# Kernel tuning notes

Hardware: AMD Instinct MI355X
Metric: run time of the kernel (lower is better)

## Reference

```python
import jax, jax.numpy as jnp
import numpy as np

HID = 16   # hidden_dim
K = 16     # kNN neighbors
B = 64     # graphs per batch
N_TS = 8192
N_LC = 12288


def setup_inputs() -> dict:
    key = jax.random.key(0)
    ks = jax.random.split(key, 24)

    def lin(k, fan_in, fan_out):
        w = jax.random.normal(k, (fan_in, fan_out), jnp.float32) / np.sqrt(fan_in).astype(np.float32)
        return w

    inp = {
        "x_ts": jax.random.normal(ks[0], (N_TS, 6), jnp.float32),
        "x_lc": jax.random.normal(ks[1], (N_LC, 5), jnp.float32),
        # balanced sorted graph ids -> every graph has >= K source nodes
        "batch_ts": jnp.repeat(jnp.arange(B, dtype=jnp.int32), N_TS // B),
        "batch_lc": jnp.repeat(jnp.arange(B, dtype=jnp.int32), N_LC // B),
        # ts_encode: Linear(6,16), ELU, Linear(16,16), ELU
        "ts_w1": lin(ks[2], 6, HID),  "ts_b1": jnp.zeros((HID,), jnp.float32),
        "ts_w2": lin(ks[3], HID, HID), "ts_b2": jnp.zeros((HID,), jnp.float32),
        # lc_encode: Linear(5,16), ELU, Linear(16,16), ELU
        "lc_w1": lin(ks[4], 5, HID),  "lc_b1": jnp.zeros((HID,), jnp.float32),
        "lc_w2": lin(ks[5], HID, HID), "lc_b2": jnp.zeros((HID,), jnp.float32),
        # EdgeConv nn: Linear(2*16, 16), ELU  (shared across the 3 conv calls)
        "conv_w": lin(ks[6], 2 * HID, HID), "conv_b": jnp.zeros((HID,), jnp.float32),
        # output MLP 16->64->32->8->4->1 (ELU between, none after last)
        "out_w1": lin(ks[7], HID, 64), "out_b1": jnp.zeros((64,), jnp.float32),
        "out_w2": lin(ks[8], 64, 32),  "out_b2": jnp.zeros((32,), jnp.float32),
        "out_w3": lin(ks[9], 32, 8),   "out_b3": jnp.zeros((8,), jnp.float32),
        "out_w4": lin(ks[10], 8, 4),   "out_b4": jnp.zeros((4,), jnp.float32),
        "out_w5": lin(ks[11], 4, 1),   "out_b5": jnp.zeros((1,), jnp.float32),
    }
    return inp


def _mlp2(x, w1, b1, w2, b2):
    return jax.nn.elu(jax.nn.elu(x @ w1 + b1) @ w2 + b2)


def _edge_conv(x_src, x_dst, b_src, b_dst, w, b):
    """DynamicEdgeConv: per-graph kNN of dst queries into src, message
    nn(cat[x_i, x_j - x_i]), max-aggregate over the K neighbors."""
    # squared distances [N_dst, N_src]
    d2 = (jnp.sum(x_dst * x_dst, 1)[:, None]
          - 2.0 * (x_dst @ x_src.T)
          + jnp.sum(x_src * x_src, 1)[None, :])
    d2 = jnp.where(b_dst[:, None] == b_src[None, :], d2, jnp.inf)
    _, idx = jax.lax.top_k(-d2, K)          # [N_dst, K] nearest (incl. self when src==dst)
    xj = x_src[idx]                          # [N_dst, K, H] gather
    xi = x_dst[:, None, :]                   # [N_dst, 1, H]
    msg = jnp.concatenate([jnp.broadcast_to(xi, xj.shape), xj - xi], axis=-1)
    msg = jax.nn.elu(msg @ w + b)            # [N_dst, K, H]
    return jnp.max(msg, axis=1)              # max aggregation -> [N_dst, H]


def reference(x_ts, x_lc, batch_ts, batch_lc,
              ts_w1, ts_b1, ts_w2, ts_b2,
              lc_w1, lc_b1, lc_w2, lc_b2,
              conv_w, conv_b,
              out_w1, out_b1, out_w2, out_b2, out_w3, out_b3,
              out_w4, out_b4, out_w5, out_b5):
    x_ts_enc = _mlp2(x_ts, ts_w1, ts_b1, ts_w2, ts_b2)   # [N_ts, 16]
    x_lc_enc = _mlp2(x_lc, lc_w1, lc_b1, lc_w2, lc_b2)   # [N_lc, 16]

    feats1 = _edge_conv(x_lc_enc, x_lc_enc, batch_lc, batch_lc, conv_w, conv_b)  # [N_lc,16]
    feats2 = _edge_conv(x_lc_enc, x_ts_enc, batch_lc, batch_ts, conv_w, conv_b)  # [N_ts,16]
    feats3 = _edge_conv(feats1,   feats2,   batch_lc, batch_ts, conv_w, conv_b)  # [N_ts,16]

    # avg_pool_x(batch_ts, feats3, batch_ts): per-graph mean
    sums = jax.ops.segment_sum(feats3, batch_ts, num_segments=B)
    cnts = jax.ops.segment_sum(jnp.ones((feats3.shape[0],), feats3.dtype), batch_ts, num_segments=B)
    pooled = sums / cnts[:, None]                         # [B, 16]

    h = jax.nn.elu(pooled @ out_w1 + out_b1)
    h = jax.nn.elu(h @ out_w2 + out_b2)
    h = jax.nn.elu(h @ out_w3 + out_b3)
    h = jax.nn.elu(h @ out_w4 + out_b4)
    out = h @ out_w5 + out_b5                             # [B, 1]
    batch_out = jnp.arange(B, dtype=batch_ts.dtype)
    return (out, batch_out)
```

## Files before the change

kernel.cpp:

```cpp
#include <hip/hip_runtime.h>
#include <math.h>

#define HID 16
#define KNN 16
#define NB 64
#define NTS 8192
#define NLC 12288
#define TSG 128
#define LCG 192

__device__ __forceinline__ float eluf(float x) {
    return x > 0.0f ? x : expm1f(x);
}

__device__ __forceinline__ unsigned int f2ord(float f) {
    unsigned int b = __float_as_uint(f);
    return b ^ (((int)b >> 31) | 0x80000000u);
}

__global__ __launch_bounds__(256) void encode_kernel(
    const float* __restrict__ x_ts, const float* __restrict__ x_lc,
    const float* __restrict__ ts_w1, const float* __restrict__ ts_b1,
    const float* __restrict__ ts_w2, const float* __restrict__ ts_b2,
    const float* __restrict__ lc_w1, const float* __restrict__ lc_b1,
    const float* __restrict__ lc_w2, const float* __restrict__ lc_b2,
    const float* __restrict__ cw,
    float* __restrict__ ts_enc, float* __restrict__ lc_enc,
    float* __restrict__ y_lc, float* __restrict__ n_lc,
    float* __restrict__ pooled)
{
    __shared__ float sw1[6 * HID];
    __shared__ float sw2[HID * HID];
    __shared__ float scw2[HID * HID];
    __shared__ float sb1[HID];
    __shared__ float sb2[HID];
    __shared__ float s_h[64 * 17];

    const int tid = threadIdx.x;
    const int t = blockIdx.x * 256 + tid;
    if (t < NB * HID) pooled[t] = 0.0f;

    const bool is_ts = (blockIdx.x < NTS / 64);
    const float* w1 = is_ts ? ts_w1 : lc_w1;
    const float* b1 = is_ts ? ts_b1 : lc_b1;
    const float* w2 = is_ts ? ts_w2 : lc_w2;
    const float* b2 = is_ts ? ts_b2 : lc_b2;
    const int in_dim = is_ts ? 6 : 5;

    if (tid < in_dim * HID) sw1[tid] = w1[tid];
    if (tid < HID * HID)    sw2[tid] = w2[tid];
    if (!is_ts && tid < HID * HID) scw2[tid] = cw[HID * HID + tid];
    if (tid < HID)          { sb1[tid] = b1[tid]; sb2[tid] = b2[tid]; }
    __syncthreads();

    const int q    = tid & 3;
    const int rloc = tid >> 2;
    const int row  = is_ts ? (blockIdx.x * 64 + rloc)
                           : ((blockIdx.x - 128) * 64 + rloc);
    const float* x = is_ts ? (x_ts + (size_t)row * 6) : (x_lc + (size_t)row * 5);
    float* outp    = is_ts ? (ts_enc + (size_t)row * HID) : (lc_enc + (size_t)row * HID);

    float xin[6];
    for (int k = 0; k < in_dim; ++k) xin[k] = x[k];

    #pragma unroll
    for (int jc = 0; jc < 4; ++jc) {
        const int c = 4 * q + jc;
        float s = sb1[c];
        for (int k = 0; k < in_dim; ++k) s += xin[k] * sw1[k * HID + c];
        s_h[rloc * 17 + c] = eluf(s);
    }
    __syncthreads();
    float hf[HID];
    #pragma unroll
    for (int k = 0; k < HID; ++k) hf[k] = s_h[rloc * 17 + k];

    float o4v[4];
    #pragma unroll
    for (int jc = 0; jc < 4; ++jc) {
        const int c = 4 * q + jc;
        float s = sb2[c];
        #pragma unroll
        for (int k = 0; k < HID; ++k) s += hf[k] * sw2[k * HID + c];
        o4v[jc] = eluf(s);
    }
    reinterpret_cast<float4*>(outp)[q] = make_float4(o4v[0], o4v[1], o4v[2], o4v[3]);

    if (!is_ts) {
        __syncthreads();
        #pragma unroll
        for (int jc = 0; jc < 4; ++jc) s_h[rloc * 17 + 4 * q + jc] = o4v[jc];
        __syncthreads();
        float of[HID];
        #pragma unroll
        for (int k = 0; k < HID; ++k) of[k] = s_h[rloc * 17 + k];
        float nv = 0.f;
        #pragma unroll
        for (int c = 0; c < HID; ++c) nv += of[c] * of[c];
        float y4[4];
        #pragma unroll
        for (int jc = 0; jc < 4; ++jc) {
            const int c = 4 * q + jc;
            float s = 0.f;
            #pragma unroll
            for (int k = 0; k < HID; ++k) s += of[k] * scw2[k * HID + c];
            y4[jc] = s;
        }
        reinterpret_cast<float4*>(y_lc + (size_t)row * HID)[q] =
            make_float4(y4[0], y4[1], y4[2], y4[3]);
        if (q == 0) n_lc[row] = nv;
    }
}

#define CONV_SMEM_FLOATS (LCG * HID + 2 * HID * HID + 2 * HID)
#define CONV_SMEM_BYTES  (CONV_SMEM_FLOATS * 4)

template<int NSRC, int NDST, bool POOL, bool EPI, bool SELF>
__device__ __forceinline__ void edgeconv_impl(
    float* __restrict__ smem, int bid,
    const float* __restrict__ src, const float* __restrict__ src_y,
    const float* __restrict__ src_n, const float* __restrict__ dst,
    const float* __restrict__ cw, const float* __restrict__ cb,
    float* __restrict__ out_feats, float* __restrict__ out_y,
    float* __restrict__ out_n, float* __restrict__ pool_out)
{
    constexpr int RPW = 2;
    constexpr int RPB = 8 * RPW;
    constexpr int BPG = NDST / RPB;
    float* s_y    = smem;
    float* s_dw   = s_y + NSRC * HID;
    float* s_w2   = s_dw + HID * HID;
    float* s_b    = s_w2 + HID * HID;
    float* s_pool = s_b + HID;

    const int tid  = threadIdx.x;
    const int lane = tid & 63;
    const int wave = tid >> 6;
    const int g      = bid / BPG;
    const int rowblk = bid % BPG;

    if (tid < HID * HID) {
        float w1v = cw[tid];
        float w2v = cw[HID * HID + tid];
        s_dw[tid] = w1v - w2v;
        if (EPI) s_w2[tid] = w2v;
    }
    if (tid < HID) s_b[tid] = cb[tid];
    if (POOL && tid < HID) s_pool[tid] = 0.0f;
    {
        const float4* gy = reinterpret_cast<const float4*>(src_y + (size_t)(g * NSRC) * HID);
        float4* sy4 = reinterpret_cast<float4*>(s_y);
        for (int i = tid; i < NSRC * HID / 4; i += 512) sy4[i] = gy[i];
    }

    float rw[3][HID];
    float rn[3];
    #pragma unroll
    for (int k = 0; k < 3; ++k) {
        const float4* rp = reinterpret_cast<const float4*>(src + (size_t)(g * NSRC + lane + 64 * k) * HID);
        float4 a = rp[0], b = rp[1], c4 = rp[2], e = rp[3];
        rw[k][0] = a.x;  rw[k][1] = a.y;  rw[k][2]  = a.z;  rw[k][3]  = a.w;
        rw[k][4] = b.x;  rw[k][5] = b.y;  rw[k][6]  = b.z;  rw[k][7]  = b.w;
        rw[k][8] = c4.x; rw[k][9] = c4.y; rw[k][10] = c4.z; rw[k][11] = c4.w;
        rw[k][12] = e.x; rw[k][13] = e.y; rw[k][14] = e.z;  rw[k][15] = e.w;
        rn[k] = src_n[g * NSRC + lane + 64 * k];
    }

    const int drow0 = rowblk * RPB + wave * RPW;
    const int c = lane & 15;

    for (int r2 = 0; r2 < RPW; ++r2) {
        const int drow = drow0 + r2;

        const float4* d4 = reinterpret_cast<const float4*>(dst + (size_t)(g * NDST + drow) * HID);
        float xi[HID];
        {
            float4 a = d4[0], b = d4[1], c4 = d4[2], e = d4[3];
            xi[0] = a.x;  xi[1] = a.y;  xi[2]  = a.z;  xi[3]  = a.w;
            xi[4] = b.x;  xi[5] = b.y;  xi[6]  = b.z;  xi[7]  = b.w;
            xi[8] = c4.x; xi[9] = c4.y; xi[10] = c4.z; xi[11] = c4.w;
            xi[12] = e.x; xi[13] = e.y; xi[14] = e.z;  xi[15] = e.w;
        }
        float nd;
        if (SELF) {
            nd = src_n[g * NSRC + drow];
        } else {
            float s = 0.f;
            #pragma unroll
            for (int cc = 0; cc < HID; ++cc) s += xi[cc] * xi[cc];
            nd = s;
        }

        unsigned int dk0, dk1, dk2;
        {
            unsigned int dk[3];
            #pragma unroll
            for (int k = 0; k < 3; ++k) {
                float dot = 0.f;
                #pragma unroll
                for (int cc = 0; cc < HID; ++cc) dot += xi[cc] * rw[k][cc];
                dk[k] = f2ord(nd - 2.0f * dot + rn[k]);
            }
            dk0 = dk[0]; dk1 = dk[1]; dk2 = dk[2];
        }

        unsigned int p = 0;
        int k = KNN;
        int cls = 3 * 64;
        int b = 31;
        for (; b >= 0; --b) {
            if (cls == k) break;
            unsigned int pb = p >> b;
            int cnt = __popcll(__ballot((dk0 >> b) == pb))
                    + __popcll(__ballot((dk1 >> b) == pb))
                    + __popcll(__ballot((dk2 >> b) == pb));
            if (k > cnt) { k -= cnt; p |= (1u << b); cls -= cnt; }
            else cls = cnt;
        }
        unsigned int qi = 255u;
        if (b >= 0) {
            p |= (1u << (b + 1)) - 1u;
        } else if (cls != k) {
            qi = 0;
            int kk = k;
            const unsigned int i0 = (unsigned)lane, i1 = (unsigned)(lane + 64), i2 = (unsigned)(lane + 128);
            for (int bb = 7; bb >= 0; --bb) {
                unsigned int qb = qi >> bb;
                int cnt = __popcll(__ballot(dk0 == p && (i0 >> bb) == qb))
                        + __popcll(__ballot(dk1 == p && (i1 >> bb) == qb))
                        + __popcll(__ballot(dk2 == p && (i2 >> bb) == qb));
                if (kk > cnt) { kk -= cnt; qi |= (1u << bb); }
            }
        }
        unsigned long long m0 = __ballot(dk0 < p || (dk0 == p && (unsigned)lane <= qi));
        unsigned long long m1 = __ballot(dk1 < p || (dk1 == p && (unsigned)(lane + 64) <= qi));
        unsigned long long m2 = __ballot(dk2 < p || (dk2 == p && (unsigned)(lane + 128) <= qi));

        if (r2 == 0) __syncthreads();

        float cic = s_b[c];
        #pragma unroll
        for (int r = 0; r < HID; ++r) cic += xi[r] * s_dw[r * HID + c];

        int jarr[KNN];
        #pragma unroll
        for (int i = 0; i < KNN; ++i) {
            int j;
            if (m0)      { j = __builtin_ctzll(m0);       m0 &= m0 - 1; }
            else if (m1) { j = 64 + __builtin_ctzll(m1);  m1 &= m1 - 1; }
            else         { j = 128 + __builtin_ctzll(m2); m2 &= m2 - 1; }
            jarr[i] = j;
        }
        float yv[KNN];
        #pragma unroll
        for (int i = 0; i < KNN; ++i) yv[i] = s_y[jarr[i] * HID + c];
        float ym = yv[0];
        #pragma unroll
        for (int i = 1; i < KNN; ++i) ym = fmaxf(ym, yv[i]);

        const float f = eluf(cic + ym);

        if (POOL) {
            if (lane < HID) atomicAdd(&s_pool[c], f);
        } else {
            const int grow = g * NDST + drow;
            if (lane < HID) out_feats[(size_t)grow * HID + c] = f;
            if (EPI) {
                float yvv = 0.f, nv = 0.f;
                #pragma unroll
                for (int r = 0; r < HID; ++r) {
                    float fr = __shfl(f, r, 64);
                    yvv += fr * s_w2[r * HID + c];
                    nv += fr * fr;
                }
                if (lane < HID) out_y[(size_t)grow * HID + c] = yvv;
                if (lane == 0)  out_n[grow] = nv;
            }
        }
    }

    if (POOL) {
        __syncthreads();
        if (tid < HID) atomicAdd(&pool_out[g * HID + tid], s_pool[tid]);
    }
}

#define C1_BLOCKS (NB * (LCG / 16))
#define C2_BLOCKS (NB * (TSG / 16))
__global__ __launch_bounds__(512) void edgeconv12_kernel(
    const float* __restrict__ lc_enc, const float* __restrict__ y_lc,
    const float* __restrict__ n_lc, const float* __restrict__ ts_enc,
    const float* __restrict__ cw, const float* __restrict__ cb,
    float* __restrict__ feats1, float* __restrict__ y_f1, float* __restrict__ n_f1,
    float* __restrict__ feats2)
{
    extern __shared__ float smem[];
    if (blockIdx.x < C1_BLOCKS)
        edgeconv_impl<LCG, LCG, false, true, true>(smem, blockIdx.x, lc_enc, y_lc, n_lc,
                                                   lc_enc, cw, cb, feats1, y_f1, n_f1, nullptr);
    else
        edgeconv_impl<LCG, TSG, false, false, false>(smem, blockIdx.x - C1_BLOCKS, lc_enc, y_lc, n_lc,
                                                     ts_enc, cw, cb, feats2, nullptr, nullptr, nullptr);
}

__global__ __launch_bounds__(512) void edgeconv3_kernel(
    const float* __restrict__ feats1, const float* __restrict__ y_f1,
    const float* __restrict__ n_f1, const float* __restrict__ feats2,
    const float* __restrict__ cw, const float* __restrict__ cb,
    float* __restrict__ pooled)
{
    extern __shared__ float smem[];
    edgeconv_impl<LCG, TSG, true, false, false>(smem, blockIdx.x, feats1, y_f1, n_f1,
                                                feats2, cw, cb, nullptr, nullptr, nullptr, pooled);
}

__global__ __launch_bounds__(64) void head_kernel(
    const float* __restrict__ pooled,
    const float* __restrict__ w1, const float* __restrict__ b1,
    const float* __restrict__ w2, const float* __restrict__ b2,
    const float* __restrict__ w3, const float* __restrict__ b3,
    const float* __restrict__ w4, const float* __restrict__ b4,
    const float* __restrict__ w5, const float* __restrict__ b5,
    float* __restrict__ out)
{
    const int g = blockIdx.x;
    const int lane = threadIdx.x;
    __shared__ float sp[HID];
    __shared__ float sh1[64];
    __shared__ float sh2[32];
    __shared__ float sh3[8];
    __shared__ float sh4[4];

    if (lane < HID) sp[lane] = pooled[g * HID + lane] * (1.0f / (float)TSG);
    __syncthreads();

    {
        float s = b1[lane];
        #pragma unroll
        for (int r = 0; r < HID; ++r) s += sp[r] * w1[r * 64 + lane];
        sh1[lane] = eluf(s);
    }
    __syncthreads();
    if (lane < 32) {
        float s = b2[lane];
        #pragma unroll
        for (int r = 0; r < 64; ++r) s += sh1[r] * w2[r * 32 + lane];
        sh2[lane] = eluf(s);
    }
    __syncthreads();
    if (lane < 8) {
        float s = b3[lane];
        #pragma unroll
        for (int r = 0; r < 32; ++r) s += sh2[r] * w3[r * 8 + lane];
        sh3[lane] = eluf(s);
    }
    __syncthreads();
    if (lane < 4) {
        float s = b4[lane];
        #pragma unroll
        for (int r = 0; r < 8; ++r) s += sh3[r] * w4[r * 4 + lane];
        sh4[lane] = eluf(s);
    }
    __syncthreads();
    if (lane == 0) {
        float s = b5[0];
        #pragma unroll
        for (int r = 0; r < 4; ++r) s += sh4[r] * w5[r];
        out[g] = s;
        out[NB + g] = (float)g;
    }
}

extern "C" void kernel_launch(void* const* d_in, const int* in_sizes, int n_in,
                              void* d_out, int out_size, void* d_ws, size_t ws_size,
                              hipStream_t stream) {
    const float* x_ts  = (const float*)d_in[0];
    const float* x_lc  = (const float*)d_in[1];
    const float* ts_w1 = (const float*)d_in[4];
    const float* ts_b1 = (const float*)d_in[5];
    const float* ts_w2 = (const float*)d_in[6];
    const float* ts_b2 = (const float*)d_in[7];
    const float* lc_w1 = (const float*)d_in[8];
    const float* lc_b1 = (const float*)d_in[9];
    const float* lc_w2 = (const float*)d_in[10];
    const float* lc_b2 = (const float*)d_in[11];
    const float* cw    = (const float*)d_in[12];
    const float* cb    = (const float*)d_in[13];
    const float* ow1   = (const float*)d_in[14];
    const float* ob1   = (const float*)d_in[15];
    const float* ow2   = (const float*)d_in[16];
    const float* ob2   = (const float*)d_in[17];
    const float* ow3   = (const float*)d_in[18];
    const float* ob3   = (const float*)d_in[19];
    const float* ow4   = (const float*)d_in[20];
    const float* ob4   = (const float*)d_in[21];
    const float* ow5   = (const float*)d_in[22];
    const float* ob5   = (const float*)d_in[23];
    float* out = (float*)d_out;

    float* ws = (float*)d_ws;
    float* ts_enc = ws;
    float* lc_enc = ws + 131072;
    float* feats1 = ws + 327680;
    float* feats2 = ws + 524288;
    float* pooled = ws + 655360;
    float* y_lc   = ws + 656384;
    float* n_lc   = ws + 852992;
    float* y_f1   = ws + 865280;
    float* n_f1   = ws + 1061888;

    encode_kernel<<<(NTS + NLC) / 64, 256, 0, stream>>>(
        x_ts, x_lc, ts_w1, ts_b1, ts_w2, ts_b2, lc_w1, lc_b1, lc_w2, lc_b2,
        cw, ts_enc, lc_enc, y_lc, n_lc, pooled);

    edgeconv12_kernel<<<C1_BLOCKS + C2_BLOCKS, 512, CONV_SMEM_BYTES, stream>>>(
        lc_enc, y_lc, n_lc, ts_enc, cw, cb, feats1, y_f1, n_f1, feats2);

    edgeconv3_kernel<<<C2_BLOCKS, 512, CONV_SMEM_BYTES, stream>>>(
        feats1, y_f1, n_f1, feats2, cw, cb, pooled);

    head_kernel<<<NB, 64, 0, stream>>>(
        pooled, ow1, ob1, ow2, ob2, ow3, ob3, ow4, ob4, ow5, ob5, out);
}
```

Baseline: 156.1 us.

## Fuse node encoders into edgeconv kernel, recomputing per-graph encodings in shared memory

Drops the separate encode kernel. Each edgeconv block for convs 1 and 2 now recomputes its graph's 192 lc encodings (plus norms and y projections) and its 16 ts destination rows directly into shared memory, then runs kNN from shared memory. This removes one launch and the global round-trip of the encoded features, at the cost of redundant encoder work: every one of the 12 or 8 blocks per graph recomputes the same lc encodings. Conv3 is unrolled into its own specialized kernel, and the pooled buffer is now zeroed by block 0.

```diff
diff --git a/kernel.cpp b/kernel.cpp
--- a/kernel.cpp
+++ b/kernel.cpp
@@ -18,120 +18,35 @@
     return b ^ (((int)b >> 31) | 0x80000000u);
 }
 
-__global__ __launch_bounds__(256) void encode_kernel(
+
+struct FusedSmem {
+    float enc[LCG * 17];
+    float y[LCG * 17];
+    float n[LCG];
+    float dw[HID * HID];
+    float cw2[HID * HID];
+    float b[HID];
+    float w1lc[5 * HID]; float b1lc[HID]; float w2lc[HID * HID]; float b2lc[HID];
+    float w1ts[6 * HID]; float b1ts[HID]; float w2ts[HID * HID]; float b2ts[HID];
+    float dst[16 * 17];
+};
+
+template<bool IS_C1>
+__device__ __forceinline__ void fused_impl(
+    FusedSmem& sm, int bid,
     const float* __restrict__ x_ts, const float* __restrict__ x_lc,
     const float* __restrict__ ts_w1, const float* __restrict__ ts_b1,
     const float* __restrict__ ts_w2, const float* __restrict__ ts_b2,
     const float* __restrict__ lc_w1, const float* __restrict__ lc_b1,
     const float* __restrict__ lc_w2, const float* __restrict__ lc_b2,
-    const float* __restrict__ cw,
-    float* __restrict__ ts_enc, float* __restrict__ lc_enc,
-    float* __restrict__ y_lc, float* __restrict__ n_lc,
-    float* __restrict__ pooled)
-{
-    __shared__ float sw1[6 * HID];
-    __shared__ float sw2[HID * HID];
-    __shared__ float scw2[HID * HID];
-    __shared__ float sb1[HID];
-    __shared__ float sb2[HID];
-    __shared__ float s_h[64 * 17];
-
-    const int tid = threadIdx.x;
-    const int t = blockIdx.x * 256 + tid;
-    if (t < NB * HID) pooled[t] = 0.0f;
-
-    const bool is_ts = (blockIdx.x < NTS / 64);
-    const float* w1 = is_ts ? ts_w1 : lc_w1;
-    const float* b1 = is_ts ? ts_b1 : lc_b1;
-    const float* w2 = is_ts ? ts_w2 : lc_w2;
-    const float* b2 = is_ts ? ts_b2 : lc_b2;
-    const int in_dim = is_ts ? 6 : 5;
-
-    if (tid < in_dim * HID) sw1[tid] = w1[tid];
-    if (tid < HID * HID)    sw2[tid] = w2[tid];
-    if (!is_ts && tid < HID * HID) scw2[tid] = cw[HID * HID + tid];
-    if (tid < HID)          { sb1[tid] = b1[tid]; sb2[tid] = b2[tid]; }
-    __syncthreads();
-
-    const int q    = tid & 3;
-    const int rloc = tid >> 2;
-    const int row  = is_ts ? (blockIdx.x * 64 + rloc)
-                           : ((blockIdx.x - 128) * 64 + rloc);
-    const float* x = is_ts ? (x_ts + (size_t)row * 6) : (x_lc + (size_t)row * 5);
-    float* outp    = is_ts ? (ts_enc + (size_t)row * HID) : (lc_enc + (size_t)row * HID);
-
-    float xin[6];
-    for (int k = 0; k < in_dim; ++k) xin[k] = x[k];
-
-    #pragma unroll
-    for (int jc = 0; jc < 4; ++jc) {
-        const int c = 4 * q + jc;
-        float s = sb1[c];
-        for (int k = 0; k < in_dim; ++k) s += xin[k] * sw1[k * HID + c];
-        s_h[rloc * 17 + c] = eluf(s);
-    }
-    __syncthreads();
-    float hf[HID];
-    #pragma unroll
-    for (int k = 0; k < HID; ++k) hf[k] = s_h[rloc * 17 + k];
-
-    float o4v[4];
-    #pragma unroll
-    for (int jc = 0; jc < 4; ++jc) {
-        const int c = 4 * q + jc;
-        float s = sb2[c];
-        #pragma unroll
-        for (int k = 0; k < HID; ++k) s += hf[k] * sw2[k * HID + c];
-        o4v[jc] = eluf(s);
-    }
-    reinterpret_cast<float4*>(outp)[q] = make_float4(o4v[0], o4v[1], o4v[2], o4v[3]);
-
-    if (!is_ts) {
-        __syncthreads();
-        #pragma unroll
-        for (int jc = 0; jc < 4; ++jc) s_h[rloc * 17 + 4 * q + jc] = o4v[jc];
-        __syncthreads();
-        float of[HID];
-        #pragma unroll
-        for (int k = 0; k < HID; ++k) of[k] = s_h[rloc * 17 + k];
-        float nv = 0.f;
-        #pragma unroll
-        for (int c = 0; c < HID; ++c) nv += of[c] * of[c];
-        float y4[4];
-        #pragma unroll
-        for (int jc = 0; jc < 4; ++jc) {
-            const int c = 4 * q + jc;
-            float s = 0.f;
-            #pragma unroll
-            for (int k = 0; k < HID; ++k) s += of[k] * scw2[k * HID + c];
-            y4[jc] = s;
-        }
-        reinterpret_cast<float4*>(y_lc + (size_t)row * HID)[q] =
-            make_float4(y4[0], y4[1], y4[2], y4[3]);
-        if (q == 0) n_lc[row] = nv;
-    }
-}
-
-#define CONV_SMEM_FLOATS (LCG * HID + 2 * HID * HID + 2 * HID)
-#define CONV_SMEM_BYTES  (CONV_SMEM_FLOATS * 4)
-
-template<int NSRC, int NDST, bool POOL, bool EPI, bool SELF>
-__device__ __forceinline__ void edgeconv_impl(
-    float* __restrict__ smem, int bid,
-    const float* __restrict__ src, const float* __restrict__ src_y,
-    const float* __restrict__ src_n, const float* __restrict__ dst,
     const float* __restrict__ cw, const float* __restrict__ cb,
     float* __restrict__ out_feats, float* __restrict__ out_y,
-    float* __restrict__ out_n, float* __restrict__ pool_out)
+    float* __restrict__ out_n)
 {
+    constexpr int NDST = IS_C1 ? LCG : TSG;
     constexpr int RPW = 2;
     constexpr int RPB = 8 * RPW;
     constexpr int BPG = NDST / RPB;
-    float* s_y    = smem;
-    float* s_dw   = s_y + NSRC * HID;
-    float* s_w2   = s_dw + HID * HID;
-    float* s_b    = s_w2 + HID * HID;
-    float* s_pool = s_b + HID;
 
     const int tid  = threadIdx.x;
     const int lane = tid & 63;
@@ -140,30 +55,86 @@
     const int rowblk = bid % BPG;
 
     if (tid < HID * HID) {
-        float w1v = cw[tid];
-        float w2v = cw[HID * HID + tid];
-        s_dw[tid] = w1v - w2v;
-        if (EPI) s_w2[tid] = w2v;
-    }
-    if (tid < HID) s_b[tid] = cb[tid];
-    if (POOL && tid < HID) s_pool[tid] = 0.0f;
-    {
-        const float4* gy = reinterpret_cast<const float4*>(src_y + (size_t)(g * NSRC) * HID);
-        float4* sy4 = reinterpret_cast<float4*>(s_y);
-        for (int i = tid; i < NSRC * HID / 4; i += 512) sy4[i] = gy[i];
-    }
+        float w1v = cw[tid], w2v = cw[HID * HID + tid];
+        sm.dw[tid]  = w1v - w2v;
+        sm.cw2[tid] = w2v;
+        sm.w2lc[tid] = lc_w2[tid];
+        if (!IS_C1) sm.w2ts[tid] = ts_w2[tid];
+    }
+    if (tid < 5 * HID) sm.w1lc[tid] = lc_w1[tid];
+    if (!IS_C1 && tid < 6 * HID) sm.w1ts[tid] = ts_w1[tid];
+    if (tid < HID) {
+        sm.b1lc[tid] = lc_b1[tid]; sm.b2lc[tid] = lc_b2[tid]; sm.b[tid] = cb[tid];
+        if (!IS_C1) { sm.b1ts[tid] = ts_b1[tid]; sm.b2ts[tid] = ts_b2[tid]; }
+    }
+    __syncthreads();
+
+    if (tid < LCG) {
+        const int r = tid;
+        const float* xp = x_lc + (size_t)(g * LCG + r) * 5;
+        float xin[5];
+        #pragma unroll
+        for (int k = 0; k < 5; ++k) xin[k] = xp[k];
+        float h[HID];
+        #pragma unroll
+        for (int c = 0; c < HID; ++c) {
+            float s = sm.b1lc[c];
+            #pragma unroll
+            for (int k = 0; k < 5; ++k) s += xin[k] * sm.w1lc[k * HID + c];
+            h[c] = eluf(s);
+        }
+        float o[HID];
+        #pragma unroll
+        for (int c = 0; c < HID; ++c) {
+            float s = sm.b2lc[c];
+            #pragma unroll
+            for (int k = 0; k < HID; ++k) s += h[k] * sm.w2lc[k * HID + c];
+            o[c] = eluf(s);
+            sm.enc[r * 17 + c] = o[c];
+        }
+        float nv = 0.f;
+        #pragma unroll
+        for (int c = 0; c < HID; ++c) nv += o[c] * o[c];
+        sm.n[r] = nv;
+        #pragma unroll
+        for (int c = 0; c < HID; ++c) {
+            float s = 0.f;
+            #pragma unroll
+            for (int k = 0; k < HID; ++k) s += o[k] * sm.cw2[k * HID + c];
+            sm.y[r * 17 + c] = s;
+        }
+    }
+    if (!IS_C1 && tid >= LCG && tid < LCG + 16) {
+        const int i = tid - LCG;
+        const float* xp = x_ts + (size_t)(g * TSG + rowblk * 16 + i) * 6;
+        float xin[6];
+        #pragma unroll
+        for (int k = 0; k < 6; ++k) xin[k] = xp[k];
+        float h[HID];
+        #pragma unroll
+        for (int c = 0; c < HID; ++c) {
+            float s = sm.b1ts[c];
+            #pragma unroll
+            for (int k = 0; k < 6; ++k) s += xin[k] * sm.w1ts[k * HID + c];
+            h[c] = eluf(s);
+        }
+        #pragma unroll
+        for (int c = 0; c < HID; ++c) {
+            float s = sm.b2ts[c];
+            #pragma unroll
+            for (int k = 0; k < HID; ++k) s += h[k] * sm.w2ts[k * HID + c];
+            sm.dst[i * 17 + c] = eluf(s);
+        }
+    }
+    __syncthreads();
 
     float rw[3][HID];
     float rn[3];
     #pragma unroll
     for (int k = 0; k < 3; ++k) {
-        const float4* rp = reinterpret_cast<const float4*>(src + (size_t)(g * NSRC + lane + 64 * k) * HID);
-        float4 a = rp[0], b = rp[1], c4 = rp[2], e = rp[3];
-        rw[k][0] = a.x;  rw[k][1] = a.y;  rw[k][2]  = a.z;  rw[k][3]  = a.w;
-        rw[k][4] = b.x;  rw[k][5] = b.y;  rw[k][6]  = b.z;  rw[k][7]  = b.w;
-        rw[k][8] = c4.x; rw[k][9] = c4.y; rw[k][10] = c4.z; rw[k][11] = c4.w;
-        rw[k][12] = e.x; rw[k][13] = e.y; rw[k][14] = e.z;  rw[k][15] = e.w;
-        rn[k] = src_n[g * NSRC + lane + 64 * k];
+        #pragma unroll
+        for (int c = 0; c < HID; ++c) rw[k][c] = sm.enc[(lane + 64 * k) * 17 + c];
+        rn[k] = sm.n[lane + 64 * k];
     }
 
     const int drow0 = rowblk * RPB + wave * RPW;
@@ -172,18 +143,18 @@
     for (int r2 = 0; r2 < RPW; ++r2) {
         const int drow = drow0 + r2;
 
-        const float4* d4 = reinterpret_cast<const float4*>(dst + (size_t)(g * NDST + drow) * HID);
         float xi[HID];
-        {
-            float4 a = d4[0], b = d4[1], c4 = d4[2], e = d4[3];
-            xi[0] = a.x;  xi[1] = a.y;  xi[2]  = a.z;  xi[3]  = a.w;
-            xi[4] = b.x;  xi[5] = b.y;  xi[6]  = b.z;  xi[7]  = b.w;
-            xi[8] = c4.x; xi[9] = c4.y; xi[10] = c4.z; xi[11] = c4.w;
-            xi[12] = e.x; xi[13] = e.y; xi[14] = e.z;  xi[15] = e.w;
+        if (IS_C1) {
+            #pragma unroll
+            for (int cc = 0; cc < HID; ++cc) xi[cc] = sm.enc[drow * 17 + cc];
+        } else {
+            const int dl = wave * RPW + r2;
+            #pragma unroll
+            for (int cc = 0; cc < HID; ++cc) xi[cc] = sm.dst[dl * 17 + cc];
         }
         float nd;
-        if (SELF) {
-            nd = src_n[g * NSRC + drow];
+        if (IS_C1) {
+            nd = sm.n[drow];
         } else {
             float s = 0.f;
             #pragma unroll
@@ -236,11 +207,9 @@
         unsigned long long m1 = __ballot(dk1 < p || (dk1 == p && (unsigned)(lane + 64) <= qi));
         unsigned long long m2 = __ballot(dk2 < p || (dk2 == p && (unsigned)(lane + 128) <= qi));
 
-        if (r2 == 0) __syncthreads();
-
-        float cic = s_b[c];
-        #pragma unroll
-        for (int r = 0; r < HID; ++r) cic += xi[r] * s_dw[r * HID + c];
+        float cic = sm.b[c];
+        #pragma unroll
+        for (int r = 0; r < HID; ++r) cic += xi[r] * sm.dw[r * HID + c];
 
         int jarr[KNN];
         #pragma unroll
@@ -253,55 +222,56 @@
         }
         float yv[KNN];
         #pragma unroll
-        for (int i = 0; i < KNN; ++i) yv[i] = s_y[jarr[i] * HID + c];
+        for (int i = 0; i < KNN; ++i) yv[i] = sm.y[jarr[i] * 17 + c];
         float ym = yv[0];
         #pragma unroll
         for (int i = 1; i < KNN; ++i) ym = fmaxf(ym, yv[i]);
 
         const float f = eluf(cic + ym);
 
-        if (POOL) {
-            if (lane < HID) atomicAdd(&s_pool[c], f);
-        } else {
-            const int grow = g * NDST + drow;
-            if (lane < HID) out_feats[(size_t)grow * HID + c] = f;
-            if (EPI) {
-                float yvv = 0.f, nv = 0.f;
-                #pragma unroll
-                for (int r = 0; r < HID; ++r) {
-                    float fr = __shfl(f, r, 64);
-                    yvv += fr * s_w2[r * HID + c];
-                    nv += fr * fr;
-                }
-                if (lane < HID) out_y[(size_t)grow * HID + c] = yvv;
-                if (lane == 0)  out_n[grow] = nv;
+        const int grow = g * NDST + drow;
+        if (lane < HID) out_feats[(size_t)grow * HID + c] = f;
+        if (IS_C1) {
+            float yvv = 0.f, nv = 0.f;
+            #pragma unroll
+            for (int r = 0; r < HID; ++r) {
+                float fr = __shfl(f, r, 64);
+                yvv += fr * sm.cw2[r * HID + c];
+                nv += fr * fr;
             }
-        }
-    }
-
-    if (POOL) {
-        __syncthreads();
-        if (tid < HID) atomicAdd(&pool_out[g * HID + tid], s_pool[tid]);
-    }
-}
-
-#define C1_BLOCKS (NB * (LCG / 16))
-#define C2_BLOCKS (NB * (TSG / 16))
-__global__ __launch_bounds__(512) void edgeconv12_kernel(
-    const float* __restrict__ lc_enc, const float* __restrict__ y_lc,
-    const float* __restrict__ n_lc, const float* __restrict__ ts_enc,
+            if (lane < HID) out_y[(size_t)grow * HID + c] = yvv;
+            if (lane == 0)  out_n[grow] = nv;
+        }
+    }
+}
+
+#define F1_BLOCKS (NB * (LCG / 16))
+#define F2_BLOCKS (NB * (TSG / 16))
+__global__ __launch_bounds__(512) void fused12_kernel(
+    const float* __restrict__ x_ts, const float* __restrict__ x_lc,
+    const float* __restrict__ ts_w1, const float* __restrict__ ts_b1,
+    const float* __restrict__ ts_w2, const float* __restrict__ ts_b2,
+    const float* __restrict__ lc_w1, const float* __restrict__ lc_b1,
+    const float* __restrict__ lc_w2, const float* __restrict__ lc_b2,
     const float* __restrict__ cw, const float* __restrict__ cb,
     float* __restrict__ feats1, float* __restrict__ y_f1, float* __restrict__ n_f1,
-    float* __restrict__ feats2)
+    float* __restrict__ feats2, float* __restrict__ pooled)
 {
-    extern __shared__ float smem[];
-    if (blockIdx.x < C1_BLOCKS)
-        edgeconv_impl<LCG, LCG, false, true, true>(smem, blockIdx.x, lc_enc, y_lc, n_lc,
-                                                   lc_enc, cw, cb, feats1, y_f1, n_f1, nullptr);
+    __shared__ FusedSmem sm;
+    if (blockIdx.x == 0) {
+        pooled[threadIdx.x] = 0.0f;
+        pooled[512 + threadIdx.x] = 0.0f;
+    }
+    if (blockIdx.x < F1_BLOCKS)
+        fused_impl<true>(sm, blockIdx.x, x_ts, x_lc, ts_w1, ts_b1, ts_w2, ts_b2,
+                         lc_w1, lc_b1, lc_w2, lc_b2, cw, cb, feats1, y_f1, n_f1);
     else
-        edgeconv_impl<LCG, TSG, false, false, false>(smem, blockIdx.x - C1_BLOCKS, lc_enc, y_lc, n_lc,
-                                                     ts_enc, cw, cb, feats2, nullptr, nullptr, nullptr);
-}
+        fused_impl<false>(sm, blockIdx.x - F1_BLOCKS, x_ts, x_lc, ts_w1, ts_b1, ts_w2, ts_b2,
+                          lc_w1, lc_b1, lc_w2, lc_b2, cw, cb, feats2, nullptr, nullptr);
+}
+
+#define CONV_SMEM_FLOATS (LCG * HID + 2 * HID * HID + 2 * HID)
+#define CONV_SMEM_BYTES  (CONV_SMEM_FLOATS * 4)
 
 __global__ __launch_bounds__(512) void edgeconv3_kernel(
     const float* __restrict__ feats1, const float* __restrict__ y_f1,
@@ -310,8 +280,142 @@
     float* __restrict__ pooled)
 {
     extern __shared__ float smem[];
-    edgeconv_impl<LCG, TSG, true, false, false>(smem, blockIdx.x, feats1, y_f1, n_f1,
-                                                feats2, cw, cb, nullptr, nullptr, nullptr, pooled);
+    constexpr int NSRC = LCG, NDST = TSG;
+    constexpr int RPW = 2;
+    constexpr int RPB = 8 * RPW;
+    constexpr int BPG = NDST / RPB;
+    float* s_y    = smem;
+    float* s_dw   = s_y + NSRC * HID;
+    float* s_w2   = s_dw + HID * HID;
+    float* s_b    = s_w2 + HID * HID;
+    float* s_pool = s_b + HID;
+
+    const int bid  = blockIdx.x;
+    const int tid  = threadIdx.x;
+    const int lane = tid & 63;
+    const int wave = tid >> 6;
+    const int g      = bid / BPG;
+    const int rowblk = bid % BPG;
+
+    if (tid < HID * HID) s_dw[tid] = cw[tid] - cw[HID * HID + tid];
+    if (tid < HID) s_b[tid] = cb[tid];
+    if (tid < HID) s_pool[tid] = 0.0f;
+    {
+        const float4* gy = reinterpret_cast<const float4*>(y_f1 + (size_t)(g * NSRC) * HID);
+        float4* sy4 = reinterpret_cast<float4*>(s_y);
+        for (int i = tid; i < NSRC * HID / 4; i += 512) sy4[i] = gy[i];
+    }
+
+    float rw[3][HID];
+    float rn[3];
+    #pragma unroll
+    for (int k = 0; k < 3; ++k) {
+        const float4* rp = reinterpret_cast<const float4*>(feats1 + (size_t)(g * NSRC + lane + 64 * k) * HID);
+        float4 a = rp[0], b = rp[1], c4 = rp[2], e = rp[3];
+        rw[k][0] = a.x;  rw[k][1] = a.y;  rw[k][2]  = a.z;  rw[k][3]  = a.w;
+        rw[k][4] = b.x;  rw[k][5] = b.y;  rw[k][6]  = b.z;  rw[k][7]  = b.w;
+        rw[k][8] = c4.x; rw[k][9] = c4.y; rw[k][10] = c4.z; rw[k][11] = c4.w;
+        rw[k][12] = e.x; rw[k][13] = e.y; rw[k][14] = e.z;  rw[k][15] = e.w;
+        rn[k] = n_f1[g * NSRC + lane + 64 * k];
+    }
+
+    const int drow0 = rowblk * RPB + wave * RPW;
+    const int c = lane & 15;
+
+    for (int r2 = 0; r2 < RPW; ++r2) {
+        const int drow = drow0 + r2;
+
+        const float4* d4 = reinterpret_cast<const float4*>(feats2 + (size_t)(g * NDST + drow) * HID);
+        float xi[HID];
+        {
+            float4 a = d4[0], b = d4[1], c4 = d4[2], e = d4[3];
+            xi[0] = a.x;  xi[1] = a.y;  xi[2]  = a.z;  xi[3]  = a.w;
+            xi[4] = b.x;  xi[5] = b.y;  xi[6]  = b.z;  xi[7]  = b.w;
+            xi[8] = c4.x; xi[9] = c4.y; xi[10] = c4.z; xi[11] = c4.w;
+            xi[12] = e.x; xi[13] = e.y; xi[14] = e.z;  xi[15] = e.w;
+        }
+        float nd;
+        {
+            float s = 0.f;
+            #pragma unroll
+            for (int cc = 0; cc < HID; ++cc) s += xi[cc] * xi[cc];
+            nd = s;
+        }
+
+        unsigned int dk0, dk1, dk2;
+        {
+            unsigned int dk[3];
+            #pragma unroll
+            for (int k = 0; k < 3; ++k) {
+                float dot = 0.f;
+                #pragma unroll
+                for (int cc = 0; cc < HID; ++cc) dot += xi[cc] * rw[k][cc];
+                dk[k] = f2ord(nd - 2.0f * dot + rn[k]);
+            }
+            dk0 = dk[0]; dk1 = dk[1]; dk2 = dk[2];
+        }
+
+        unsigned int p = 0;
+        int k = KNN;
+        int cls = 3 * 64;
+        int b = 31;
+        for (; b >= 0; --b) {
+            if (cls == k) break;
+            unsigned int pb = p >> b;
+            int cnt = __popcll(__ballot((dk0 >> b) == pb))
+                    + __popcll(__ballot((dk1 >> b) == pb))
+                    + __popcll(__ballot((dk2 >> b) == pb));
+            if (k > cnt) { k -= cnt; p |= (1u << b); cls -= cnt; }
+            else cls = cnt;
+        }
+        unsigned int qi = 255u;
+        if (b >= 0) {
+            p |= (1u << (b + 1)) - 1u;
+        } else if (cls != k) {
+            qi = 0;
+            int kk = k;
+            const unsigned int i0 = (unsigned)lane, i1 = (unsigned)(lane + 64), i2 = (unsigned)(lane + 128);
+            for (int bb = 7; bb >= 0; --bb) {
+                unsigned int qb = qi >> bb;
+                int cnt = __popcll(__ballot(dk0 == p && (i0 >> bb) == qb))
+                        + __popcll(__ballot(dk1 == p && (i1 >> bb) == qb))
+                        + __popcll(__ballot(dk2 == p && (i2 >> bb) == qb));
+                if (kk > cnt) { kk -= cnt; qi |= (1u << bb); }
+            }
+        }
+        unsigned long long m0 = __ballot(dk0 < p || (dk0 == p && (unsigned)lane <= qi));
+        unsigned long long m1 = __ballot(dk1 < p || (dk1 == p && (unsigned)(lane + 64) <= qi));
+        unsigned long long m2 = __ballot(dk2 < p || (dk2 == p && (unsigned)(lane + 128) <= qi));
+
+        if (r2 == 0) __syncthreads();
+
+        float cic = s_b[c];
+        #pragma unroll
+        for (int r = 0; r < HID; ++r) cic += xi[r] * s_dw[r * HID + c];
+
+        int jarr[KNN];
+        #pragma unroll
+        for (int i = 0; i < KNN; ++i) {
+            int j;
+            if (m0)      { j = __builtin_ctzll(m0);       m0 &= m0 - 1; }
+            else if (m1) { j = 64 + __builtin_ctzll(m1);  m1 &= m1 - 1; }
+            else         { j = 128 + __builtin_ctzll(m2); m2 &= m2 - 1; }
+            jarr[i] = j;
+        }
+        float yv[KNN];
+        #pragma unroll
+        for (int i = 0; i < KNN; ++i) yv[i] = s_y[jarr[i] * HID + c];
+        float ym = yv[0];
+        #pragma unroll
+        for (int i = 1; i < KNN; ++i) ym = fmaxf(ym, yv[i]);
+
+        const float f = eluf(cic + ym);
+
+        if (lane < HID) atomicAdd(&s_pool[c], f);
+    }
+
+    __syncthreads();
+    if (tid < HID) atomicAdd(&pooled[g * HID + tid], s_pool[tid]);
 }
 
 __global__ __launch_bounds__(64) void head_kernel(
@@ -399,24 +503,17 @@
     float* out = (float*)d_out;
 
     float* ws = (float*)d_ws;
-    float* ts_enc = ws;
-    float* lc_enc = ws + 131072;
-    float* feats1 = ws + 327680;
-    float* feats2 = ws + 524288;
-    float* pooled = ws + 655360;
-    float* y_lc   = ws + 656384;
-    float* n_lc   = ws + 852992;
-    float* y_f1   = ws + 865280;
-    float* n_f1   = ws + 1061888;
-
-    encode_kernel<<<(NTS + NLC) / 64, 256, 0, stream>>>(
+    float* feats1 = ws;
+    float* feats2 = ws + 196608;
+    float* y_f1   = ws + 327680;
+    float* n_f1   = ws + 524288;
+    float* pooled = ws + 536576;
+
+    fused12_kernel<<<F1_BLOCKS + F2_BLOCKS, 512, 0, stream>>>(
         x_ts, x_lc, ts_w1, ts_b1, ts_w2, ts_b2, lc_w1, lc_b1, lc_w2, lc_b2,
-        cw, ts_enc, lc_enc, y_lc, n_lc, pooled);
-
-    edgeconv12_kernel<<<C1_BLOCKS + C2_BLOCKS, 512, CONV_SMEM_BYTES, stream>>>(
-        lc_enc, y_lc, n_lc, ts_enc, cw, cb, feats1, y_f1, n_f1, feats2);
-
-    edgeconv3_kernel<<<C2_BLOCKS, 512, CONV_SMEM_BYTES, stream>>>(
+        cw, cb, feats1, y_f1, n_f1, feats2, pooled);
+
+    edgeconv3_kernel<<<F2_BLOCKS, 512, CONV_SMEM_BYTES, stream>>>(
         feats1, y_f1, n_f1, feats2, cw, cb, pooled);
 
     head_kernel<<<NB, 64, 0, stream>>>(
```

New measurement: 171.8 us. +10.1%, slower.

## Skip common radix-select prefix bits and compact kNN indices via mbcnt into LDS

Applied to the files above, without the earlier changes.

Before the bitwise radix select for the k-th smallest distance, the wave computes an AND/OR reduction over all keys to find the highest differing bit, so the ballot loop starts there instead of bit 31. The serial ctz-based extraction of 16 neighbor indices from the ballot masks is replaced with an mbcnt prefix-rank scatter into a per-wave LDS index buffer, which is then read back. This removes many scalar/ballot iterations but adds 12 cross-lane shuffles and extra LDS traffic. It relies on wave-local LDS ordering without a barrier, which holds within a single wave.

```diff
diff --git a/kernel.cpp b/kernel.cpp
--- a/kernel.cpp
+++ b/kernel.cpp
@@ -112,7 +112,7 @@
     }
 }
 
-#define CONV_SMEM_FLOATS (LCG * HID + 2 * HID * HID + 2 * HID)
+#define CONV_SMEM_FLOATS (LCG * HID + 2 * HID * HID + 2 * HID + 8 * KNN)
 #define CONV_SMEM_BYTES  (CONV_SMEM_FLOATS * 4)
 
 template<int NSRC, int NDST, bool POOL, bool EPI, bool SELF>
@@ -132,6 +132,7 @@
     float* s_w2   = s_dw + HID * HID;
     float* s_b    = s_w2 + HID * HID;
     float* s_pool = s_b + HID;
+    int*   s_widx = (int*)(s_pool + HID);
 
     const int tid  = threadIdx.x;
     const int lane = tid & 63;
@@ -168,6 +169,7 @@
 
     const int drow0 = rowblk * RPB + wave * RPW;
     const int c = lane & 15;
+    const int wbase = wave * KNN;
 
     for (int r2 = 0; r2 < RPW; ++r2) {
         const int drow = drow0 + r2;
@@ -204,10 +206,27 @@
             dk0 = dk[0]; dk1 = dk[1]; dk2 = dk[2];
         }
 
-        unsigned int p = 0;
+        unsigned int a_and = dk0 & dk1 & dk2;
+        unsigned int a_or  = dk0 | dk1 | dk2;
+        #pragma unroll
+        for (int ofs = 1; ofs < 64; ofs <<= 1) {
+            a_and &= (unsigned int)__shfl_xor((int)a_and, ofs, 64);
+            a_or  |= (unsigned int)__shfl_xor((int)a_or,  ofs, 64);
+        }
+        unsigned int diff = a_and ^ a_or;
+        int b;
+        unsigned int p;
+        if (diff == 0) {
+            b = -1; p = a_and;
+        } else {
+            b = 31 - __builtin_clz(diff);
+            p = a_and & ~((2u << b) - 1u);
+        }
+        b = __builtin_amdgcn_readfirstlane(b);
+        p = (unsigned int)__builtin_amdgcn_readfirstlane((int)p);
+
         int k = KNN;
         int cls = 3 * 64;
-        int b = 31;
         for (; b >= 0; --b) {
             if (cls == k) break;
             unsigned int pb = p >> b;
@@ -232,9 +251,12 @@
                 if (kk > cnt) { kk -= cnt; qi |= (1u << bb); }
             }
         }
-        unsigned long long m0 = __ballot(dk0 < p || (dk0 == p && (unsigned)lane <= qi));
-        unsigned long long m1 = __ballot(dk1 < p || (dk1 == p && (unsigned)(lane + 64) <= qi));
-        unsigned long long m2 = __ballot(dk2 < p || (dk2 == p && (unsigned)(lane + 128) <= qi));
+        const bool in0 = dk0 < p || (dk0 == p && (unsigned)lane <= qi);
+        const bool in1 = dk1 < p || (dk1 == p && (unsigned)(lane + 64) <= qi);
+        const bool in2 = dk2 < p || (dk2 == p && (unsigned)(lane + 128) <= qi);
+        unsigned long long m0 = __ballot(in0);
+        unsigned long long m1 = __ballot(in1);
+        unsigned long long m2 = __ballot(in2);
 
         if (r2 == 0) __syncthreads();
 
@@ -242,18 +264,25 @@
         #pragma unroll
         for (int r = 0; r < HID; ++r) cic += xi[r] * s_dw[r * HID + c];
 
-        int jarr[KNN];
+        {
+            int r0 = __builtin_amdgcn_mbcnt_lo((unsigned int)(m0 & 0xFFFFFFFFu), 0);
+            r0 = __builtin_amdgcn_mbcnt_hi((unsigned int)(m0 >> 32), r0);
+            int r1 = __builtin_amdgcn_mbcnt_lo((unsigned int)(m1 & 0xFFFFFFFFu), 0);
+            r1 = __builtin_amdgcn_mbcnt_hi((unsigned int)(m1 >> 32), r1);
+            int r2m = __builtin_amdgcn_mbcnt_lo((unsigned int)(m2 & 0xFFFFFFFFu), 0);
+            r2m = __builtin_amdgcn_mbcnt_hi((unsigned int)(m2 >> 32), r2m);
+            const int n0 = __popcll(m0);
+            const int n01 = n0 + __popcll(m1);
+            if (in0) s_widx[wbase + r0]        = lane;
+            if (in1) s_widx[wbase + n0 + r1]   = lane + 64;
+            if (in2) s_widx[wbase + n01 + r2m] = lane + 128;
+        }
+        float yv[KNN];
         #pragma unroll
         for (int i = 0; i < KNN; ++i) {
-            int j;
-            if (m0)      { j = __builtin_ctzll(m0);       m0 &= m0 - 1; }
-            else if (m1) { j = 64 + __builtin_ctzll(m1);  m1 &= m1 - 1; }
-            else         { j = 128 + __builtin_ctzll(m2); m2 &= m2 - 1; }
-            jarr[i] = j;
-        }
-        float yv[KNN];
-        #pragma unroll
-        for (int i = 0; i < KNN; ++i) yv[i] = s_y[jarr[i] * HID + c];
+            const int j = s_widx[wbase + i];
+            yv[i] = s_y[j * HID + c];
+        }
         float ym = yv[0];
         #pragma unroll
         for (int i = 1; i < KNN; ++i) ym = fmaxf(ym, yv[i]);
```

Measured after the change: 161.8 us. 1.04x slower.

## Process one dst row per wave and remap blocks so graphs stay on one XCD

Applied to the files above, without the earlier changes.

Each wave now handles one destination row instead of two, which doubles the number of blocks. A new block-index mapping places all blocks of a graph on the same XCD (bid&7), so each graph's source data stays in one L2. The intent is more parallelism plus better L2 locality. The cost is that per-block setup (loading the source tile into shared memory and registers) is now amortised over half as many rows.

```diff
diff --git a/kernel.cpp b/kernel.cpp
--- a/kernel.cpp
+++ b/kernel.cpp
@@ -117,16 +117,13 @@
 
 template<int NSRC, int NDST, bool POOL, bool EPI, bool SELF>
 __device__ __forceinline__ void edgeconv_impl(
-    float* __restrict__ smem, int bid,
+    float* __restrict__ smem, int g, int rowblk,
     const float* __restrict__ src, const float* __restrict__ src_y,
     const float* __restrict__ src_n, const float* __restrict__ dst,
     const float* __restrict__ cw, const float* __restrict__ cb,
     float* __restrict__ out_feats, float* __restrict__ out_y,
     float* __restrict__ out_n, float* __restrict__ pool_out)
 {
-    constexpr int RPW = 2;
-    constexpr int RPB = 8 * RPW;
-    constexpr int BPG = NDST / RPB;
     float* s_y    = smem;
     float* s_dw   = s_y + NSRC * HID;
     float* s_w2   = s_dw + HID * HID;
@@ -136,8 +133,6 @@
     const int tid  = threadIdx.x;
     const int lane = tid & 63;
     const int wave = tid >> 6;
-    const int g      = bid / BPG;
-    const int rowblk = bid % BPG;
 
     if (tid < HID * HID) {
         float w1v = cw[tid];
@@ -166,127 +161,126 @@
         rn[k] = src_n[g * NSRC + lane + 64 * k];
     }
 
-    const int drow0 = rowblk * RPB + wave * RPW;
+    const int drow = rowblk * 8 + wave;
+    const float4* d4 = reinterpret_cast<const float4*>(dst + (size_t)(g * NDST + drow) * HID);
+    float xi[HID];
+    {
+        float4 a = d4[0], b = d4[1], c4 = d4[2], e = d4[3];
+        xi[0] = a.x;  xi[1] = a.y;  xi[2]  = a.z;  xi[3]  = a.w;
+        xi[4] = b.x;  xi[5] = b.y;  xi[6]  = b.z;  xi[7]  = b.w;
+        xi[8] = c4.x; xi[9] = c4.y; xi[10] = c4.z; xi[11] = c4.w;
+        xi[12] = e.x; xi[13] = e.y; xi[14] = e.z;  xi[15] = e.w;
+    }
+    float nd;
+    if (SELF) {
+        nd = src_n[g * NSRC + drow];
+    } else {
+        float s = 0.f;
+        #pragma unroll
+        for (int c = 0; c < HID; ++c) s += xi[c] * xi[c];
+        nd = s;
+    }
+
+    unsigned int dk0, dk1, dk2;
+    {
+        unsigned int dk[3];
+        #pragma unroll
+        for (int k = 0; k < 3; ++k) {
+            float dot = 0.f;
+            #pragma unroll
+            for (int c = 0; c < HID; ++c) dot += xi[c] * rw[k][c];
+            dk[k] = f2ord(nd - 2.0f * dot + rn[k]);
+        }
+        dk0 = dk[0]; dk1 = dk[1]; dk2 = dk[2];
+    }
+
+    unsigned int p = 0;
+    int k = KNN;
+    int cls = 3 * 64;
+    int b = 31;
+    for (; b >= 0; --b) {
+        if (cls == k) break;
+        unsigned int pb = p >> b;
+        int cnt = __popcll(__ballot((dk0 >> b) == pb))
+                + __popcll(__ballot((dk1 >> b) == pb))
+                + __popcll(__ballot((dk2 >> b) == pb));
+        if (k > cnt) { k -= cnt; p |= (1u << b); cls -= cnt; }
+        else cls = cnt;
+    }
+    unsigned int qi = 255u;
+    if (b >= 0) {
+        p |= (1u << (b + 1)) - 1u;
+    } else if (cls != k) {
+        qi = 0;
+        int kk = k;
+        const unsigned int i0 = (unsigned)lane, i1 = (unsigned)(lane + 64), i2 = (unsigned)(lane + 128);
+        for (int bb = 7; bb >= 0; --bb) {
+            unsigned int qb = qi >> bb;
+            int cnt = __popcll(__ballot(dk0 == p && (i0 >> bb) == qb))
+                    + __popcll(__ballot(dk1 == p && (i1 >> bb) == qb))
+                    + __popcll(__ballot(dk2 == p && (i2 >> bb) == qb));
+            if (kk > cnt) { kk -= cnt; qi |= (1u << bb); }
+        }
+    }
+    unsigned long long m0 = __ballot(dk0 < p || (dk0 == p && (unsigned)lane <= qi));
+    unsigned long long m1 = __ballot(dk1 < p || (dk1 == p && (unsigned)(lane + 64) <= qi));
+    unsigned long long m2 = __ballot(dk2 < p || (dk2 == p && (unsigned)(lane + 128) <= qi));
+
+    __syncthreads();
+
     const int c = lane & 15;
-
-    for (int r2 = 0; r2 < RPW; ++r2) {
-        const int drow = drow0 + r2;
-
-        const float4* d4 = reinterpret_cast<const float4*>(dst + (size_t)(g * NDST + drow) * HID);
-        float xi[HID];
-        {
-            float4 a = d4[0], b = d4[1], c4 = d4[2], e = d4[3];
-            xi[0] = a.x;  xi[1] = a.y;  xi[2]  = a.z;  xi[3]  = a.w;
-            xi[4] = b.x;  xi[5] = b.y;  xi[6]  = b.z;  xi[7]  = b.w;
-            xi[8] = c4.x; xi[9] = c4.y; xi[10] = c4.z; xi[11] = c4.w;
-            xi[12] = e.x; xi[13] = e.y; xi[14] = e.z;  xi[15] = e.w;
-        }
-        float nd;
-        if (SELF) {
-            nd = src_n[g * NSRC + drow];
-        } else {
-            float s = 0.f;
-            #pragma unroll
-            for (int cc = 0; cc < HID; ++cc) s += xi[cc] * xi[cc];
-            nd = s;
-        }
-
-        unsigned int dk0, dk1, dk2;
-        {
-            unsigned int dk[3];
-            #pragma unroll
-            for (int k = 0; k < 3; ++k) {
-                float dot = 0.f;
-                #pragma unroll
-                for (int cc = 0; cc < HID; ++cc) dot += xi[cc] * rw[k][cc];
-                dk[k] = f2ord(nd - 2.0f * dot + rn[k]);
-            }
-            dk0 = dk[0]; dk1 = dk[1]; dk2 = dk[2];
-        }
-
-        unsigned int p = 0;
-        int k = KNN;
-        int cls = 3 * 64;
-        int b = 31;
-        for (; b >= 0; --b) {
-            if (cls == k) break;
-            unsigned int pb = p >> b;
-            int cnt = __popcll(__ballot((dk0 >> b) == pb))
-                    + __popcll(__ballot((dk1 >> b) == pb))
-                    + __popcll(__ballot((dk2 >> b) == pb));
-            if (k > cnt) { k -= cnt; p |= (1u << b); cls -= cnt; }
-            else cls = cnt;
-        }
-        unsigned int qi = 255u;
-        if (b >= 0) {
-            p |= (1u << (b + 1)) - 1u;
-        } else if (cls != k) {
-            qi = 0;
-            int kk = k;
-            const unsigned int i0 = (unsigned)lane, i1 = (unsigned)(lane + 64), i2 = (unsigned)(lane + 128);
-            for (int bb = 7; bb >= 0; --bb) {
-                unsigned int qb = qi >> bb;
-                int cnt = __popcll(__ballot(dk0 == p && (i0 >> bb) == qb))
-                        + __popcll(__ballot(dk1 == p && (i1 >> bb) == qb))
-                        + __popcll(__ballot(dk2 == p && (i2 >> bb) == qb));
-                if (kk > cnt) { kk -= cnt; qi |= (1u << bb); }
-            }
-        }
-        unsigned long long m0 = __ballot(dk0 < p || (dk0 == p && (unsigned)lane <= qi));
-        unsigned long long m1 = __ballot(dk1 < p || (dk1 == p && (unsigned)(lane + 64) <= qi));
-        unsigned long long m2 = __ballot(dk2 < p || (dk2 == p && (unsigned)(lane + 128) <= qi));
-
-        if (r2 == 0) __syncthreads();
-
-        float cic = s_b[c];
-        #pragma unroll
-        for (int r = 0; r < HID; ++r) cic += xi[r] * s_dw[r * HID + c];
-
-        int jarr[KNN];
-        #pragma unroll
-        for (int i = 0; i < KNN; ++i) {
-            int j;
-            if (m0)      { j = __builtin_ctzll(m0);       m0 &= m0 - 1; }
-            else if (m1) { j = 64 + __builtin_ctzll(m1);  m1 &= m1 - 1; }
-            else         { j = 128 + __builtin_ctzll(m2); m2 &= m2 - 1; }
-            jarr[i] = j;
-        }
-        float yv[KNN];
-        #pragma unroll
-        for (int i = 0; i < KNN; ++i) yv[i] = s_y[jarr[i] * HID + c];
-        float ym = yv[0];
-        #pragma unroll
-        for (int i = 1; i < KNN; ++i) ym = fmaxf(ym, yv[i]);
-
-        const float f = eluf(cic + ym);
-
-        if (POOL) {
-            if (lane < HID) atomicAdd(&s_pool[c], f);
-        } else {
-            const int grow = g * NDST + drow;
-            if (lane < HID) out_feats[(size_t)grow * HID + c] = f;
-            if (EPI) {
-                float yvv = 0.f, nv = 0.f;
-                #pragma unroll
-                for (int r = 0; r < HID; ++r) {
-                    float fr = __shfl(f, r, 64);
-                    yvv += fr * s_w2[r * HID + c];
-                    nv += fr * fr;
-                }
-                if (lane < HID) out_y[(size_t)grow * HID + c] = yvv;
-                if (lane == 0)  out_n[grow] = nv;
-            }
-        }
-    }
+    float cic = s_b[c];
+    #pragma unroll
+    for (int r = 0; r < HID; ++r) cic += xi[r] * s_dw[r * HID + c];
+
+    int jarr[KNN];
+    #pragma unroll
+    for (int i = 0; i < KNN; ++i) {
+        int j;
+        if (m0)      { j = __builtin_ctzll(m0);       m0 &= m0 - 1; }
+        else if (m1) { j = 64 + __builtin_ctzll(m1);  m1 &= m1 - 1; }
+        else         { j = 128 + __builtin_ctzll(m2); m2 &= m2 - 1; }
+        jarr[i] = j;
+    }
+    float yv[KNN];
+    #pragma unroll
+    for (int i = 0; i < KNN; ++i) yv[i] = s_y[jarr[i] * HID + c];
+    float ym = yv[0];
+    #pragma unroll
+    for (int i = 1; i < KNN; ++i) ym = fmaxf(ym, yv[i]);
+
+    const float f = eluf(cic + ym);
 
     if (POOL) {
+        if (lane < HID) atomicAdd(&s_pool[c], f);
         __syncthreads();
         if (tid < HID) atomicAdd(&pool_out[g * HID + tid], s_pool[tid]);
-    }
-}
-
-#define C1_BLOCKS (NB * (LCG / 16))
-#define C2_BLOCKS (NB * (TSG / 16))
+    } else {
+        const int grow = g * NDST + drow;
+        if (lane < HID) out_feats[(size_t)grow * HID + c] = f;
+        if (EPI) {
+            float yvv = 0.f, nv = 0.f;
+            #pragma unroll
+            for (int r = 0; r < HID; ++r) {
+                float fr = __shfl(f, r, 64);
+                yvv += fr * s_w2[r * HID + c];
+                nv += fr * fr;
+            }
+            if (lane < HID) out_y[(size_t)grow * HID + c] = yvv;
+            if (lane == 0)  out_n[grow] = nv;
+        }
+    }
+}
+
+__device__ __forceinline__ void xcd_map(int bid, int bpg, int& g, int& rowblk) {
+    const int x = bid & 7;
+    const int y = bid >> 3;
+    g = x + 8 * (y / bpg);
+    rowblk = y % bpg;
+}
+
+#define C1_BLOCKS (NB * (LCG / 8))
+#define C2_BLOCKS (NB * (TSG / 8))
 __global__ __launch_bounds__(512) void edgeconv12_kernel(
     const float* __restrict__ lc_enc, const float* __restrict__ y_lc,
     const float* __restrict__ n_lc, const float* __restrict__ ts_enc,
@@ -295,12 +289,16 @@
     float* __restrict__ feats2)
 {
     extern __shared__ float smem[];
-    if (blockIdx.x < C1_BLOCKS)
-        edgeconv_impl<LCG, LCG, false, true, true>(smem, blockIdx.x, lc_enc, y_lc, n_lc,
+    int g, rowblk;
+    if (blockIdx.x < C1_BLOCKS) {
+        xcd_map(blockIdx.x, LCG / 8, g, rowblk);
+        edgeconv_impl<LCG, LCG, false, true, true>(smem, g, rowblk, lc_enc, y_lc, n_lc,
                                                    lc_enc, cw, cb, feats1, y_f1, n_f1, nullptr);
-    else
-        edgeconv_impl<LCG, TSG, false, false, false>(smem, blockIdx.x - C1_BLOCKS, lc_enc, y_lc, n_lc,
+    } else {
+        xcd_map(blockIdx.x - C1_BLOCKS, TSG / 8, g, rowblk);
+        edgeconv_impl<LCG, TSG, false, false, false>(smem, g, rowblk, lc_enc, y_lc, n_lc,
                                                      ts_enc, cw, cb, feats2, nullptr, nullptr, nullptr);
+    }
 }
 
 __global__ __launch_bounds__(512) void edgeconv3_kernel(
@@ -310,7 +308,9 @@
     float* __restrict__ pooled)
 {
     extern __shared__ float smem[];
-    edgeconv_impl<LCG, TSG, true, false, false>(smem, blockIdx.x, feats1, y_f1, n_f1,
+    int g, rowblk;
+    xcd_map(blockIdx.x, TSG / 8, g, rowblk);
+    edgeconv_impl<LCG, TSG, true, false, false>(smem, g, rowblk, feats1, y_f1, n_f1,
                                                 feats2, cw, cb, nullptr, nullptr, nullptr, pooled);
 }
 
```

Result: no change. 154.1 us (-1.2%).
